# Kernel optimization log

Measured on AMD Instinct MI355X. Metric: run time of the kernel, lower is better.

Reference implementation:

```python
import math
import jax, jax.numpy as jnp
import numpy as np

D_MODEL = 1024
D_STATE = 16
D_CONV = 4
EXPAND = 2
N_MOD = 2
D_INNER = EXPAND * D_MODEL
DT_RANK = math.ceil(D_MODEL / 16)
B_SZ = 2
SEQLEN = 2048


def setup_inputs() -> dict:
    key = jax.random.key(0)
    ks = jax.random.split(key, 10)
    hidden_states = jax.random.normal(ks[0], (B_SZ, SEQLEN, D_MODEL), jnp.float32)
    modality_ids = jax.random.randint(ks[1], (B_SZ, SEQLEN), 0, N_MOD).astype(jnp.int32)
    W_in = jax.random.normal(ks[2], (N_MOD, 2 * D_INNER, D_MODEL), jnp.float32) * (D_MODEL ** -0.5)
    conv_w = jax.random.normal(ks[3], (D_INNER, D_CONV), jnp.float32) * (D_CONV ** -0.5)
    conv_b = jnp.zeros((D_INNER,), jnp.float32)
    W_x = jax.random.normal(ks[4], (N_MOD, DT_RANK + 2 * D_STATE, D_INNER), jnp.float32) * (D_INNER ** -0.5)
    dt_init_std = DT_RANK ** -0.5
    W_dt = jax.random.uniform(ks[5], (N_MOD, D_INNER, DT_RANK), jnp.float32, -dt_init_std, dt_init_std)
    # dt bias init: inverse-softplus of dt ~ LogUniform(dt_min, dt_max), per Mamba
    dt = jnp.exp(jax.random.uniform(ks[6], (N_MOD, D_INNER), jnp.float32)
                 * (math.log(0.1) - math.log(0.001)) + math.log(0.001))
    dt = jnp.maximum(dt, 1e-4)
    b_dt = dt + jnp.log(-jnp.expm1(-dt))
    A_log = jnp.log(jnp.broadcast_to(jnp.arange(1, D_STATE + 1, dtype=jnp.float32), (D_INNER, D_STATE)))
    D = jnp.ones((D_INNER,), jnp.float32)
    W_out = jax.random.normal(ks[7], (N_MOD, D_MODEL, D_INNER), jnp.float32) * (D_INNER ** -0.5)
    return dict(hidden_states=hidden_states, modality_ids=modality_ids, W_in=W_in,
                conv_w=conv_w, conv_b=conv_b, W_x=W_x, W_dt=W_dt, b_dt=b_dt,
                A_log=A_log, D=D, W_out=W_out)


def _expert_apply(x, W, ids):
    # x: [T, d_in], W: [E, d_out, d_in], ids: [T] -> per-token expert output [T, d_out]
    all_out = jnp.einsum('td,eod->teo', x, W)
    return jnp.take_along_axis(all_out, ids[:, None, None], axis=1)[:, 0, :]


def _forward(hidden_states, modality_ids, W_in, conv_w, conv_b, W_x, W_dt, b_dt, A_log, D, W_out):
    Bsz, L, d_model = hidden_states.shape
    d_inner, d_state = A_log.shape
    dt_rank = W_dt.shape[2]
    d_conv = conv_w.shape[1]
    ids = modality_ids.reshape(-1)  # [T]

    # per-modality in_proj dispatch/combine
    xz = _expert_apply(hidden_states.reshape(-1, d_model), W_in, ids)  # [T, 2*d_inner]
    xz = xz.reshape(Bsz, L, 2 * d_inner).transpose(0, 2, 1)            # [B, 2*d_inner, L]
    x, z = jnp.split(xz, 2, axis=1)                                    # [B, d_inner, L] each

    # causal depthwise conv1d (pad left d_conv-1, truncate to L) + SiLU
    xp = jnp.pad(x, ((0, 0), (0, 0), (d_conv - 1, 0)))
    xc = conv_b[None, :, None]
    for k in range(d_conv):
        xc = xc + conv_w[None, :, k:k + 1] * xp[:, :, k:k + L]
    x = jax.nn.silu(xc)

    # per-modality x_proj -> (dt, B, C)
    xt = x.transpose(0, 2, 1).reshape(-1, d_inner)                     # [T, d_inner]
    x_dbl = _expert_apply(xt, W_x, ids)
    dt, Bm, Cm = jnp.split(x_dbl, [dt_rank, dt_rank + d_state], axis=-1)

    # per-modality dt_proj (with bias), then softplus (delta_softplus=True)
    dt = _expert_apply(dt, W_dt, ids) + b_dt[ids]                      # [T, d_inner]
    dt = jax.nn.softplus(dt)

    A = -jnp.exp(A_log)                                                # [d_inner, d_state]

    # selective scan over sequence (time-major)
    dts = dt.reshape(Bsz, L, d_inner).transpose(1, 0, 2)               # [L, B, d_inner]
    Bms = Bm.reshape(Bsz, L, d_state).transpose(1, 0, 2)               # [L, B, d_state]
    Cms = Cm.reshape(Bsz, L, d_state).transpose(1, 0, 2)               # [L, B, d_state]
    xs = x.transpose(2, 0, 1)                                          # [L, B, d_inner]

    def step(state, inp):
        x_t, dt_t, B_t, C_t = inp
        dA = jnp.exp(dt_t[..., None] * A)                              # [B, d_inner, d_state]
        state = state * dA + (dt_t * x_t)[..., None] * B_t[:, None, :]
        y_t = jnp.einsum('bdn,bn->bd', state, C_t)
        return state, y_t

    init = jnp.zeros((Bsz, d_inner, d_state), jnp.float32)
    _, ys = jax.lax.scan(step, init, (xs, dts, Bms, Cms))              # ys: [L, B, d_inner]

    y = ys.transpose(1, 0, 2)                                          # [B, L, d_inner]
    y = y + x.transpose(0, 2, 1) * D[None, None, :]                    # skip D*u
    y = y * jax.nn.silu(z.transpose(0, 2, 1))                          # z gate

    # per-modality out_proj
    out = _expert_apply(y.reshape(-1, d_inner), W_out, ids)
    return out.reshape(Bsz, L, d_model)


def reference(hidden_states, modality_ids, W_in, conv_w, conv_b, W_x, W_dt, b_dt, A_log, D, W_out):
    return _forward(hidden_states, modality_ids, W_in, conv_w, conv_b, W_x, W_dt, b_dt, A_log, D, W_out)
```

## Files before the change

kernel.cpp:

```cpp
#include <hip/hip_runtime.h>
#include <hip/hip_bf16.h>
#include <math.h>

#define B_SZ 2
#define SEQLEN 2048
#define D_MODEL 1024
#define D_INNER 2048
#define D_STATE 16
#define D_CONV 4
#define DT_RANK 64
#define NTOK (B_SZ * SEQLEN)
#define XDBL 96
#define NC 32
#define LC 64
#define PADTOT (17 * 256)

typedef float f32x4 __attribute__((ext_vector_type(4)));
typedef unsigned int u32x4 __attribute__((ext_vector_type(4)));
typedef __hip_bfloat16 bf16;

__device__ __forceinline__ float siluf(float v) { return v / (1.f + __expf(-v)); }
__device__ __forceinline__ float softplusf(float v) {
  return (v > 20.f) ? v : __logf(1.f + __expf(v));
}

__device__ __forceinline__ void mfma_bf16(f32x4& acc, u32x4 a, u32x4 b) {
  asm volatile("v_mfma_f32_16x16x32_bf16 %0, %1, %2, %0" : "+v"(acc) : "v"(a), "v"(b));
}

__device__ __forceinline__ void gload16(const bf16* g, bf16* l) {
  __builtin_amdgcn_global_load_lds(
      (const __attribute__((address_space(1))) unsigned int*)g,
      (__attribute__((address_space(3))) unsigned int*)l, 16, 0, 0);
}

__global__ __launch_bounds__(1024) void k_perm(const int* __restrict__ ids, int* __restrict__ perm) {
  __shared__ int sc[1024];
  const int tid = threadIdx.x;
  int loc[4];
  int cnt = 0;
#pragma unroll
  for (int q = 0; q < 4; q++) {
    loc[q] = ids[tid * 4 + q];
    cnt += (loc[q] == 0);
  }
  sc[tid] = cnt;
  __syncthreads();
  for (int off = 1; off < 1024; off <<= 1) {
    int v = sc[tid];
    int u = (tid >= off) ? sc[tid - off] : 0;
    __syncthreads();
    sc[tid] = v + u;
    __syncthreads();
  }
  const int N0 = sc[1023];
  const int m0 = (N0 + 255) & ~255;
  const int N1 = NTOK - N0;
  for (int idx = tid; idx < PADTOT; idx += 1024)
    if ((idx >= N0 && idx < m0) || idx >= m0 + N1) perm[idx] = -1;
  int zb = sc[tid] - cnt;
#pragma unroll
  for (int q = 0; q < 4; q++) {
    int t = tid * 4 + q;
    if (loc[q] == 0) { perm[zb] = t; zb++; }
    else             { perm[m0 + (t - zb)] = t; }
  }
}

#define CVT_H   (NTOK * D_MODEL)
#define CVT_WIN (2 * 2 * D_INNER * D_MODEL)
#define CVT_WX  (2 * XDBL * D_INNER)
#define CVT_WDT (2 * D_INNER * DT_RANK)
#define CVT_WO  (2 * D_MODEL * D_INNER)
#define CVT_TOT (CVT_H + CVT_WIN + CVT_WX + CVT_WDT + CVT_WO)
__global__ __launch_bounds__(256) void k_cvtall(const float* __restrict__ h,
                                                const float* __restrict__ Win,
                                                const float* __restrict__ Wx,
                                                const float* __restrict__ Wdt,
                                                const float* __restrict__ Wout,
                                                bf16* __restrict__ hB, bf16* __restrict__ WinB,
                                                bf16* __restrict__ WxB, bf16* __restrict__ WdtB,
                                                bf16* __restrict__ WoB) {
  size_t i = ((size_t)blockIdx.x * 256 + threadIdx.x) * 8;
  const float* src; bf16* dst; size_t off;
  if (i < CVT_H)                          { src = h;    dst = hB;   off = i; }
  else if (i < CVT_H + CVT_WIN)           { src = Win;  dst = WinB; off = i - CVT_H; }
  else if (i < CVT_H + CVT_WIN + CVT_WX)  { src = Wx;   dst = WxB;  off = i - CVT_H - CVT_WIN; }
  else if (i < CVT_TOT - CVT_WO)          { src = Wdt;  dst = WdtB; off = i - CVT_H - CVT_WIN - CVT_WX; }
  else                                    { src = Wout; dst = WoB;  off = i - (CVT_TOT - CVT_WO); }
  float4 f0 = *(const float4*)&src[off];
  float4 f1 = *(const float4*)&src[off + 4];
  __align__(16) bf16 tmp[8];
  tmp[0] = __float2bfloat16(f0.x); tmp[1] = __float2bfloat16(f0.y);
  tmp[2] = __float2bfloat16(f0.z); tmp[3] = __float2bfloat16(f0.w);
  tmp[4] = __float2bfloat16(f1.x); tmp[5] = __float2bfloat16(f1.y);
  tmp[6] = __float2bfloat16(f1.z); tmp[7] = __float2bfloat16(f1.w);
  *(u32x4*)&dst[off] = *(const u32x4*)tmp;
}

template <int KDIM, int NW, int KSPLIT, int EPI>
__device__ __forceinline__ void gemmP_body(const bf16* __restrict__ actB,
                                           const int* __restrict__ perm,
                                           const int* __restrict__ ids,
                                           const bf16* __restrict__ WB,
                                           bf16* __restrict__ outx,
                                           bf16* __restrict__ outz,
                                           float* __restrict__ out0) {
  constexpr int KLEN = KDIM / KSPLIT;
  constexpr int NT = KLEN / 64;
  constexpr int NCOL = (EPI == 1) ? (D_MODEL / 128) : 0;
  __shared__ bf16 As[3][256 * 64];
  __shared__ bf16 Ws[3][128 * 64];
  const int tid = threadIdx.x;

  const int gx = gridDim.x;
  const int nwg = gx * gridDim.y;
  const int fid = blockIdx.y * gx + blockIdx.x;
  const int q8 = nwg >> 3;
  const int swz = (fid & 7) * q8 + (fid >> 3);
  const int bx = swz % gx, by = swz / gx;
  const int ot = (KSPLIT > 1) ? (bx % NCOL) * 128 : bx * 128;
  const int kz = (KSPLIT > 1) ? bx / NCOL : 0;
  const int kbase = kz * KLEN;
  const int tt = by * 256;

  const int lane = tid & 63, w = tid >> 6;
  const int wr = w >> 1, wc = w & 1;
  const int lr = lane & 15, lg = lane >> 4;

  const int t00 = perm[tt];
  const int eu = (t00 >= 0) ? ids[t00] : 0;
  const size_t wexp = (size_t)eu * NW * KDIM;

  const int kswz = ((lane & 7) ^ ((lane >> 3) & 7)) * 8;
  size_t aBase[4]; int aLds[4];
  size_t bBase[2]; int bLds[2];
#pragma unroll
  for (int v = 0; v < 4; v++) {
    const int row = w * 32 + v * 8 + (lane >> 3);
    int ta = perm[tt + row]; if (ta < 0) ta = 0;
    aBase[v] = (size_t)ta * KDIM + kswz;
    aLds[v] = (w * 32 + v * 8) * 64;
  }
#pragma unroll
  for (int v = 0; v < 2; v++) {
    const int row = w * 16 + v * 8 + (lane >> 3);
    bBase[v] = wexp + (size_t)(ot + row) * KDIM + kswz;
    bLds[v] = (w * 16 + v * 8) * 64;
  }

  f32x4 acc[4][4];
#pragma unroll
  for (int i = 0; i < 4; i++)
#pragma unroll
    for (int j = 0; j < 4; j++) acc[i][j] = (f32x4){0.f, 0.f, 0.f, 0.f};

#pragma unroll
  for (int kt = 0; kt < 2; kt++) {
    const int k0 = kbase + kt * 64;
    gload16(&actB[aBase[0] + k0], &As[kt][aLds[0]]);
    gload16(&actB[aBase[1] + k0], &As[kt][aLds[1]]);
    gload16(&actB[aBase[2] + k0], &As[kt][aLds[2]]);
    gload16(&actB[aBase[3] + k0], &As[kt][aLds[3]]);
    gload16(&WB[bBase[0] + k0], &Ws[kt][bLds[0]]);
    gload16(&WB[bBase[1] + k0], &Ws[kt][bLds[1]]);
  }

  int bR = 0, bS = 2;
  for (int kt = 0; kt < NT; ++kt) {
    const int kp = kbase + (kt + 2) * 64;
    const bool st = (kt + 2 < NT);
    if (st) {
      gload16(&actB[aBase[0] + kp], &As[bS][aLds[0]]);
      gload16(&actB[aBase[1] + kp], &As[bS][aLds[1]]);
      gload16(&WB[bBase[0] + kp], &Ws[bS][bLds[0]]);
    }
    if (kt < NT - 2)       asm volatile("s_waitcnt vmcnt(9)" ::: "memory");
    else if (kt == NT - 2) asm volatile("s_waitcnt vmcnt(6)" ::: "memory");
    else                   asm volatile("s_waitcnt vmcnt(0)" ::: "memory");
    asm volatile("s_barrier" ::: "memory");

    const bf16* Ab = As[bR];
    const bf16* Wb = Ws[bR];
    u32x4 a[4][2], b0[2][2];
#pragma unroll
    for (int f = 0; f < 4; f++)
#pragma unroll
      for (int s = 0; s < 2; s++) {
        const int row = wr * 64 + f * 16 + lr;
        a[f][s] = *(const u32x4*)&Ab[row * 64 + ((s * 4 + lg) ^ (row & 7)) * 8];
      }
#pragma unroll
    for (int j = 0; j < 2; j++)
#pragma unroll
      for (int s = 0; s < 2; s++) {
        const int row = wc * 64 + j * 16 + lr;
        b0[j][s] = *(const u32x4*)&Wb[row * 64 + ((s * 4 + lg) ^ (row & 7)) * 8];
      }
    __builtin_amdgcn_s_setprio(1);
#pragma unroll
    for (int f = 0; f < 4; f++)
#pragma unroll
      for (int j = 0; j < 2; j++) {
        mfma_bf16(acc[f][j], a[f][0], b0[j][0]);
        mfma_bf16(acc[f][j], a[f][1], b0[j][1]);
      }
    __builtin_amdgcn_s_setprio(0);

    if (st) {
      gload16(&actB[aBase[2] + kp], &As[bS][aLds[2]]);
      gload16(&actB[aBase[3] + kp], &As[bS][aLds[3]]);
      gload16(&WB[bBase[1] + kp], &Ws[bS][bLds[1]]);
    }
    u32x4 b1[2][2];
#pragma unroll
    for (int j = 0; j < 2; j++)
#pragma unroll
      for (int s = 0; s < 2; s++) {
        const int row = wc * 64 + (2 + j) * 16 + lr;
        b1[j][s] = *(const u32x4*)&Wb[row * 64 + ((s * 4 + lg) ^ (row & 7)) * 8];
      }
    __builtin_amdgcn_s_setprio(1);
#pragma unroll
    for (int f = 0; f < 4; f++)
#pragma unroll
      for (int j = 0; j < 2; j++) {
        mfma_bf16(acc[f][2 + j], a[f][0], b1[j][0]);
        mfma_bf16(acc[f][2 + j], a[f][1], b1[j][1]);
      }
    __builtin_amdgcn_s_setprio(0);
    asm volatile("s_waitcnt lgkmcnt(0)" ::: "memory");
    asm volatile("s_barrier" ::: "memory");
    bR = (bR == 2) ? 0 : bR + 1;
    bS = (bS == 2) ? 0 : bS + 1;
  }

#pragma unroll
  for (int i = 0; i < 4; i++) {
#pragma unroll
    for (int r = 0; r < 4; r++) {
      const int m = wr * 64 + i * 16 + lg * 4 + r;
      const int t = perm[tt + m];
      if (t < 0) continue;
#pragma unroll
      for (int j = 0; j < 4; j++) {
        const int col = ot + wc * 64 + j * 16 + lr;
        const float v = acc[i][j][r];
        if (EPI == 0) {
          const bf16 vb = __float2bfloat16(v);
          if (col < D_INNER) outx[(size_t)t * D_INNER + col] = vb;
          else outz[(size_t)t * D_INNER + (col - D_INNER)] = vb;
        } else {
          out0[((size_t)kz * NTOK + t) * D_MODEL + col] = v;
        }
      }
    }
  }
}

__global__ __launch_bounds__(512) void k_inproj(const bf16* actB, const int* perm, const int* ids,
                                                const bf16* WB, bf16* outx, bf16* outz) {
  gemmP_body<D_MODEL, 2 * D_INNER, 1, 0>(actB, perm, ids, WB, outx, outz, nullptr);
}
__global__ __launch_bounds__(512) void k_outproj(const bf16* actB, const int* perm, const int* ids,
                                                 const bf16* WB, float* out0) {
  gemmP_body<D_INNER, D_MODEL, 2, 1>(actB, perm, ids, WB, nullptr, nullptr, out0);
}

__global__ __launch_bounds__(256) void k_xdblg(const bf16* __restrict__ actB,
                                               const int* __restrict__ perm,
                                               const int* __restrict__ ids,
                                               const bf16* __restrict__ WB,
                                               float* __restrict__ out0) {
  constexpr int KDIM = D_INNER, NW = XDBL, LDO = XDBL, KSPLIT = 8;
  constexpr int KLEN = KDIM / KSPLIT;
  __shared__ bf16 As[128 * 64];
  __shared__ bf16 Ws[128 * 64];
  __shared__ int permL[128];
  const int tid = threadIdx.x;
  const int bx = blockIdx.x, by = blockIdx.y;

  const int ot = 0;
  const int kz = bx;
  const int kbase = kz * KLEN;
  const int tt = by * 128;

  if (tid < 128) permL[tid] = perm[tt + tid];

  const int lane = tid & 63, w = tid >> 6;
  const int wr = w >> 1, wc = w & 1;
  const int lr = lane & 15, lg = lane >> 4;

  const int t00 = perm[tt];
  const int eu = (t00 >= 0) ? ids[t00] : 0;
  const size_t wexp = (size_t)eu * NW * KDIM;

  const int srow = w * 32 + (lane >> 3);
  const int scol = (lane & 7) * 8;
  size_t abase[4], bbase[4];
  int ldsoff[4];
#pragma unroll
  for (int v = 0; v < 4; v++) {
    const int row = srow + v * 8;
    int ta = perm[tt + row];
    if (ta < 0) ta = 0;
    abase[v] = (size_t)ta * KDIM + scol;
    int orow = ot + row;
    orow = (orow < NW) ? orow : (NW - 1);
    bbase[v] = wexp + (size_t)orow * KDIM + scol;
    ldsoff[v] = (w * 32 + v * 8) * 64;
  }

  f32x4 acc[4][4];
#pragma unroll
  for (int i = 0; i < 4; i++)
#pragma unroll
    for (int j = 0; j < 4; j++) acc[i][j] = (f32x4){0.f, 0.f, 0.f, 0.f};

  for (int k0 = kbase; k0 < kbase + KLEN; k0 += 64) {
#pragma unroll
    for (int v = 0; v < 4; v++) {
      gload16(&actB[abase[v] + k0], &As[ldsoff[v]]);
      gload16(&WB[bbase[v] + k0], &Ws[ldsoff[v]]);
    }
    __syncthreads();
#pragma unroll
    for (int ks = 0; ks < 64; ks += 32) {
      u32x4 a[4], b[4];
#pragma unroll
      for (int f = 0; f < 4; f++)
        a[f] = *(const u32x4*)&As[(wr * 64 + f * 16 + lr) * 64 + ks + lg * 8];
#pragma unroll
      for (int f = 0; f < 4; f++)
        b[f] = *(const u32x4*)&Ws[(wc * 64 + f * 16 + lr) * 64 + ks + lg * 8];
#pragma unroll
      for (int i = 0; i < 4; i++)
#pragma unroll
        for (int j = 0; j < 4; j++) mfma_bf16(acc[i][j], a[i], b[j]);
    }
    __syncthreads();
  }

#pragma unroll
  for (int i = 0; i < 4; i++) {
#pragma unroll
    for (int r = 0; r < 4; r++) {
      const int m = wr * 64 + i * 16 + lg * 4 + r;
      const int t = permL[m];
      if (t < 0) continue;
#pragma unroll
      for (int j = 0; j < 4; j++) {
        const int col = ot + wc * 64 + j * 16 + lr;
        if (col < NW) out0[((size_t)kz * NTOK + t) * LDO + col] = acc[i][j][r];
      }
    }
  }
}

__global__ __launch_bounds__(256, 4) void k_dtv(const float* __restrict__ xdbl,
                                                const int* __restrict__ perm,
                                                const int* __restrict__ ids,
                                                const float* __restrict__ Wdt,
                                                const float* __restrict__ bdt,
                                                bf16* __restrict__ dtB) {
  __shared__ float Xs[64][65];
  __shared__ float Ws[64][65];
  __shared__ int permL[64];
  const int tid = threadIdx.x;
  const int tt = blockIdx.y * 64;
  const int cb = blockIdx.x * 64;
  if (tid < 64) permL[tid] = perm[tt + tid];
  const int t0 = perm[tt];
  const int e = (t0 >= 0) ? ids[t0] : 0;
  {
    const int r = tid >> 2, q = (tid & 3) * 16;
    int ta = perm[tt + r];
    if (ta < 0) ta = 0;
    const float* xsrc = &xdbl[(size_t)ta * XDBL + q];
    const float* wsrc = &Wdt[((size_t)e * D_INNER + cb + r) * DT_RANK + q];
#pragma unroll
    for (int u = 0; u < 4; u++) {
      float4 xv = *(const float4*)&xsrc[u * 4];
      float4 wv = *(const float4*)&wsrc[u * 4];
      *(float4*)&Xs[r][q + u * 4] = xv;
      *(float4*)&Ws[r][q + u * 4] = wv;
    }
  }
  __syncthreads();
  const int tl = (tid & 15) * 4;
  const int cl = (tid >> 4) * 4;
  float acc[4][4] = {};
#pragma unroll 2
  for (int k4 = 0; k4 < 16; k4++) {
    float4 xv[4], wv[4];
#pragma unroll
    for (int i = 0; i < 4; i++) xv[i] = *(const float4*)&Xs[tl + i][k4 * 4];
#pragma unroll
    for (int j = 0; j < 4; j++) wv[j] = *(const float4*)&Ws[cl + j][k4 * 4];
#pragma unroll
    for (int i = 0; i < 4; i++)
#pragma unroll
      for (int j = 0; j < 4; j++) {
        acc[i][j] = fmaf(xv[i].x, wv[j].x, acc[i][j]);
        acc[i][j] = fmaf(xv[i].y, wv[j].y, acc[i][j]);
        acc[i][j] = fmaf(xv[i].z, wv[j].z, acc[i][j]);
        acc[i][j] = fmaf(xv[i].w, wv[j].w, acc[i][j]);
      }
  }
#pragma unroll
  for (int i = 0; i < 4; i++) {
    const int t = permL[tl + i];
    if (t < 0) continue;
    __align__(8) bf16 ov[4];
#pragma unroll
    for (int j = 0; j < 4; j++)
      ov[j] = __float2bfloat16(softplusf(acc[i][j] + bdt[e * D_INNER + cb + cl + j]));
    *(uint2*)&dtB[(size_t)t * D_INNER + cb + cl] = *(const uint2*)ov;
  }
}

__global__ __launch_bounds__(256) void k_xred(const float* __restrict__ part,
                                              float* __restrict__ xdbl) {
  const int i = blockIdx.x * 256 + threadIdx.x;
  float s = 0.f;
#pragma unroll
  for (int k = 0; k < 8; k++) s += part[(size_t)k * NTOK * XDBL + i];
  xdbl[i] = s;
}

__global__ __launch_bounds__(256) void k_ored2(const float* __restrict__ part,
                                               float* __restrict__ out) {
  const size_t base = ((size_t)blockIdx.x * 256 + threadIdx.x) * 4;
  constexpr size_t NM = (size_t)NTOK * D_MODEL;
  float4 s = *(const float4*)&part[base];
  float4 p = *(const float4*)&part[NM + base];
  s.x += p.x; s.y += p.y; s.z += p.z; s.w += p.w;
  *(float4*)&out[base] = s;
}

__global__ __launch_bounds__(256) void k_conv(const bf16* __restrict__ xrawB,
                                              const float* __restrict__ cw,
                                              const float* __restrict__ cb,
                                              bf16* __restrict__ xB) {
  int idx = blockIdx.x * 256 + threadIdx.x;
  int c = idx & (D_INNER - 1);
  int t = idx >> 11;
  int l = t & (SEQLEN - 1);
  int b = t >> 11;
  float acc = cb[c];
#pragma unroll
  for (int k = 0; k < D_CONV; k++) {
    int ll = l + k - (D_CONV - 1);
    if (ll >= 0)
      acc = fmaf(cw[c * D_CONV + k],
                 __bfloat162float(xrawB[((size_t)(b * SEQLEN + ll)) * D_INNER + c]), acc);
  }
  xB[(size_t)idx] = __float2bfloat16(siluf(acc));
}

__global__ __launch_bounds__(256) void k_scan_part(const bf16* __restrict__ xB,
                                                   const bf16* __restrict__ dtB,
                                                   const float* __restrict__ xdbl,
                                                   const float* __restrict__ A_log,
                                                   float* __restrict__ F,
                                                   float* __restrict__ Sdt) {
  __shared__ float Bs[LC][D_STATE];
  const int tid = threadIdx.x;
  const int j = blockIdx.y;
  const int ch = blockIdx.x * 256 + tid;
  const int b = ch >> 11, c = ch & (D_INNER - 1);
  const int t0 = (b << 11) + j * LC;
  {
    int l = tid >> 2, q = (tid & 3) * 4;
    *(float4*)&Bs[l][q] = *(const float4*)&xdbl[(size_t)(t0 + l) * XDBL + DT_RANK + q];
  }
  float Ar[D_STATE];
#pragma unroll
  for (int n4 = 0; n4 < 4; n4++) {
    float4 a = *(const float4*)&A_log[(size_t)c * D_STATE + n4 * 4];
    Ar[n4 * 4 + 0] = -__expf(a.x); Ar[n4 * 4 + 1] = -__expf(a.y);
    Ar[n4 * 4 + 2] = -__expf(a.z); Ar[n4 * 4 + 3] = -__expf(a.w);
  }
  __syncthreads();
  float st[D_STATE];
#pragma unroll
  for (int n = 0; n < D_STATE; n++) st[n] = 0.f;
  float sdt = 0.f;
  float dtc = __bfloat162float(dtB[(size_t)t0 * D_INNER + c]);
  float xc = __bfloat162float(xB[(size_t)t0 * D_INNER + c]);
  for (int l = 0; l < LC; l++) {
    float dtn = 0.f, xn = 0.f;
    if (l < LC - 1) {
      dtn = __bfloat162float(dtB[(size_t)(t0 + l + 1) * D_INNER + c]);
      xn = __bfloat162float(xB[(size_t)(t0 + l + 1) * D_INNER + c]);
    }
    const float dtx = dtc * xc;
    sdt += dtc;
#pragma unroll
    for (int n = 0; n < D_STATE; n++) {
      float dA = __expf(dtc * Ar[n]);
      st[n] = fmaf(st[n], dA, dtx * Bs[l][n]);
    }
    dtc = dtn; xc = xn;
  }
  const size_t fb = ((size_t)j * NTOK + ch) * D_STATE;
#pragma unroll
  for (int n4 = 0; n4 < 4; n4++)
    *(float4*)&F[fb + n4 * 4] = make_float4(st[n4 * 4], st[n4 * 4 + 1], st[n4 * 4 + 2], st[n4 * 4 + 3]);
  Sdt[(size_t)j * NTOK + ch] = sdt;
}

__global__ __launch_bounds__(256) void k_combine(const float* __restrict__ F,
                                                 const float* __restrict__ Sdt,
                                                 const float* __restrict__ A_log,
                                                 float* __restrict__ s0) {
  const int gid = blockIdx.x * 256 + threadIdx.x;
  const int ch = gid >> 4, n = gid & 15, c = ch & (D_INNER - 1);
  const float Ar = -__expf(A_log[(size_t)c * D_STATE + n]);
  float s = 0.f;
  for (int j = 0; j < NC; j++) {
    s0[((size_t)j * NTOK + ch) * D_STATE + n] = s;
    s = fmaf(s, __expf(Ar * Sdt[(size_t)j * NTOK + ch]), F[((size_t)j * NTOK + ch) * D_STATE + n]);
  }
}

__global__ __launch_bounds__(256) void k_scan_fin(const bf16* __restrict__ xB,
                                                  const bf16* __restrict__ dtB,
                                                  const float* __restrict__ xdbl,
                                                  const bf16* __restrict__ zB,
                                                  const float* __restrict__ A_log,
                                                  const float* __restrict__ Dp,
                                                  const float* __restrict__ s0,
                                                  bf16* __restrict__ ybuf) {
  __shared__ float Bs[LC][D_STATE];
  __shared__ float Cs[LC][D_STATE];
  const int tid = threadIdx.x;
  const int j = blockIdx.y;
  const int ch = blockIdx.x * 256 + tid;
  const int b = ch >> 11, c = ch & (D_INNER - 1);
  const int t0 = (b << 11) + j * LC;
  {
    int l = tid >> 2, q = (tid & 3) * 4;
    *(float4*)&Bs[l][q] = *(const float4*)&xdbl[(size_t)(t0 + l) * XDBL + DT_RANK + q];
    *(float4*)&Cs[l][q] = *(const float4*)&xdbl[(size_t)(t0 + l) * XDBL + DT_RANK + D_STATE + q];
  }
  float Ar[D_STATE];
#pragma unroll
  for (int n4 = 0; n4 < 4; n4++) {
    float4 a = *(const float4*)&A_log[(size_t)c * D_STATE + n4 * 4];
    Ar[n4 * 4 + 0] = -__expf(a.x); Ar[n4 * 4 + 1] = -__expf(a.y);
    Ar[n4 * 4 + 2] = -__expf(a.z); Ar[n4 * 4 + 3] = -__expf(a.w);
  }
  __syncthreads();
  float st[D_STATE];
  const size_t sb = ((size_t)j * NTOK + ch) * D_STATE;
#pragma unroll
  for (int n4 = 0; n4 < 4; n4++) {
    float4 s = *(const float4*)&s0[sb + n4 * 4];
    st[n4 * 4 + 0] = s.x; st[n4 * 4 + 1] = s.y; st[n4 * 4 + 2] = s.z; st[n4 * 4 + 3] = s.w;
  }
  const float Dc = Dp[c];
  float dtc = __bfloat162float(dtB[(size_t)t0 * D_INNER + c]);
  float xc = __bfloat162float(xB[(size_t)t0 * D_INNER + c]);
  for (int l = 0; l < LC; l++) {
    float dtn = 0.f, xn = 0.f;
    if (l < LC - 1) {
      dtn = __bfloat162float(dtB[(size_t)(t0 + l + 1) * D_INNER + c]);
      xn = __bfloat162float(xB[(size_t)(t0 + l + 1) * D_INNER + c]);
    }
    const float zv = __bfloat162float(zB[(size_t)(t0 + l) * D_INNER + c]);
    const float dtx = dtc * xc;
    float y = 0.f;
#pragma unroll
    for (int n = 0; n < D_STATE; n++) {
      float dA = __expf(dtc * Ar[n]);
      st[n] = fmaf(st[n], dA, dtx * Bs[l][n]);
      y = fmaf(st[n], Cs[l][n], y);
    }
    float yv = fmaf(xc, Dc, y);
    ybuf[(size_t)(t0 + l) * D_INNER + c] = __float2bfloat16(yv * siluf(zv));
    dtc = dtn; xc = xn;
  }
}

extern "C" void kernel_launch(void* const* d_in, const int* in_sizes, int n_in,
                              void* d_out, int out_size, void* d_ws, size_t ws_size,
                              hipStream_t stream) {
  const float* h = (const float*)d_in[0];
  const int* ids = (const int*)d_in[1];
  const float* Win = (const float*)d_in[2];
  const float* cw = (const float*)d_in[3];
  const float* cb = (const float*)d_in[4];
  const float* Wx = (const float*)d_in[5];
  const float* Wdt = (const float*)d_in[6];
  const float* bdt = (const float*)d_in[7];
  const float* Alog = (const float*)d_in[8];
  const float* Dp = (const float*)d_in[9];
  const float* Wout = (const float*)d_in[10];
  float* out = (float*)d_out;

  const size_t NTD = (size_t)NTOK * D_INNER;
  float* ws = (float*)d_ws;
  float* slot0 = ws + 0 * NTD;
  float* slot1 = ws + 1 * NTD;
  float* slot2 = ws + 2 * NTD;
  float* slot3 = ws + 3 * NTD;
  size_t cur = 4 * NTD;
  float* xdbl_p = ws + cur; cur += (size_t)NTOK * XDBL;
  float* sdt_p = ws + cur; cur += (size_t)NC * NTOK;
  int* perm = (int*)(ws + cur); cur += PADTOT;
  bf16* xB = (bf16*)(ws + cur); cur += NTD / 2;
  bf16* WoB = (bf16*)(ws + cur); cur += CVT_WO / 2;
  bf16* WxB = (bf16*)(ws + cur); cur += CVT_WX / 2;
  bf16* WdtB = (bf16*)(ws + cur); cur += CVT_WDT / 2;

  bf16* hB = (bf16*)slot0;
  bf16* dtbB = (bf16*)slot0;
  bf16* zB = (bf16*)slot1;
  bf16* WinB = (bf16*)slot2;
  float* part = slot2;
  float* part2 = slot1;
  bf16* xrawB = (bf16*)slot3;
  float* F = slot3;
  bf16* yB = (bf16*)slot3;
  float* s0 = (float*)d_out;

  k_perm<<<1, 1024, 0, stream>>>(ids, perm);
  k_cvtall<<<CVT_TOT / 8 / 256, 256, 0, stream>>>(h, Win, Wx, Wdt, Wout, hB, WinB, WxB, WdtB, WoB);
  k_inproj<<<dim3(32, 17), 512, 0, stream>>>(hB, perm, ids, WinB, xrawB, zB);
  k_conv<<<NTD / 256, 256, 0, stream>>>(xrawB, cw, cb, xB);
  k_xdblg<<<dim3(8, 34), 256, 0, stream>>>(xB, perm, ids, WxB, part);
  k_xred<<<NTOK * XDBL / 256, 256, 0, stream>>>(part, xdbl_p);
  k_dtv<<<dim3(32, PADTOT / 64), 256, 0, stream>>>(xdbl_p, perm, ids, Wdt, bdt, dtbB);
  k_scan_part<<<dim3(16, NC), 256, 0, stream>>>(xB, dtbB, xdbl_p, Alog, F, sdt_p);
  k_combine<<<256, 256, 0, stream>>>(F, sdt_p, Alog, s0);
  k_scan_fin<<<dim3(16, NC), 256, 0, stream>>>(xB, dtbB, xdbl_p, zB, Alog, Dp, s0, yB);
  k_outproj<<<dim3(16, 17), 512, 0, stream>>>(yB, perm, ids, WoB, part2);
  k_ored2<<<NTOK * D_MODEL / 4 / 256, 256, 0, stream>>>(part2, out);
}
```

Before: 321.6 us.

## Specialize out_proj GEMM with 256x256 tiles and store scan chunk states in bf16

The shared templated GEMM is split into a dedicated in_proj kernel and a new out_proj kernel. The out_proj kernel uses 256x256 output tiles, 8 waves arranged 2x4, and double buffering instead of triple, so it launches half as many workgroups and reuses each staged A tile across more columns. Separately, the chunk-final scan states and the combined chunk-start states are written and read as bf16 instead of fp32, halving that intermediate traffic. The bf16 state storage lowers the precision of the carried scan state, and the larger tile raises register and LDS pressure.

```diff
diff --git a/kernel.cpp b/kernel.cpp
--- a/kernel.cpp
+++ b/kernel.cpp
@@ -98,17 +98,15 @@
   *(u32x4*)&dst[off] = *(const u32x4*)tmp;
 }
 
-template <int KDIM, int NW, int KSPLIT, int EPI>
-__device__ __forceinline__ void gemmP_body(const bf16* __restrict__ actB,
-                                           const int* __restrict__ perm,
-                                           const int* __restrict__ ids,
-                                           const bf16* __restrict__ WB,
-                                           bf16* __restrict__ outx,
-                                           bf16* __restrict__ outz,
-                                           float* __restrict__ out0) {
-  constexpr int KLEN = KDIM / KSPLIT;
-  constexpr int NT = KLEN / 64;
-  constexpr int NCOL = (EPI == 1) ? (D_MODEL / 128) : 0;
+__global__ __launch_bounds__(512) void k_inproj(const bf16* __restrict__ actB,
+                                                const int* __restrict__ perm,
+                                                const int* __restrict__ ids,
+                                                const bf16* __restrict__ WB,
+                                                bf16* __restrict__ outx,
+                                                bf16* __restrict__ outz) {
+  constexpr int KDIM = D_MODEL;
+  constexpr int NW = 2 * D_INNER;
+  constexpr int NT = KDIM / 64;
   __shared__ bf16 As[3][256 * 64];
   __shared__ bf16 Ws[3][128 * 64];
   const int tid = threadIdx.x;
@@ -119,9 +117,7 @@
   const int q8 = nwg >> 3;
   const int swz = (fid & 7) * q8 + (fid >> 3);
   const int bx = swz % gx, by = swz / gx;
-  const int ot = (KSPLIT > 1) ? (bx % NCOL) * 128 : bx * 128;
-  const int kz = (KSPLIT > 1) ? bx / NCOL : 0;
-  const int kbase = kz * KLEN;
+  const int ot = bx * 128;
   const int tt = by * 256;
 
   const int lane = tid & 63, w = tid >> 6;
@@ -157,7 +153,7 @@
 
 #pragma unroll
   for (int kt = 0; kt < 2; kt++) {
-    const int k0 = kbase + kt * 64;
+    const int k0 = kt * 64;
     gload16(&actB[aBase[0] + k0], &As[kt][aLds[0]]);
     gload16(&actB[aBase[1] + k0], &As[kt][aLds[1]]);
     gload16(&actB[aBase[2] + k0], &As[kt][aLds[2]]);
@@ -168,7 +164,7 @@
 
   int bR = 0, bS = 2;
   for (int kt = 0; kt < NT; ++kt) {
-    const int kp = kbase + (kt + 2) * 64;
+    const int kp = (kt + 2) * 64;
     const bool st = (kt + 2 < NT);
     if (st) {
       gload16(&actB[aBase[0] + kp], &As[bS][aLds[0]]);
@@ -245,26 +241,127 @@
 #pragma unroll
       for (int j = 0; j < 4; j++) {
         const int col = ot + wc * 64 + j * 16 + lr;
-        const float v = acc[i][j][r];
-        if (EPI == 0) {
-          const bf16 vb = __float2bfloat16(v);
-          if (col < D_INNER) outx[(size_t)t * D_INNER + col] = vb;
-          else outz[(size_t)t * D_INNER + (col - D_INNER)] = vb;
-        } else {
-          out0[((size_t)kz * NTOK + t) * D_MODEL + col] = v;
-        }
-      }
-    }
-  }
-}
-
-__global__ __launch_bounds__(512) void k_inproj(const bf16* actB, const int* perm, const int* ids,
-                                                const bf16* WB, bf16* outx, bf16* outz) {
-  gemmP_body<D_MODEL, 2 * D_INNER, 1, 0>(actB, perm, ids, WB, outx, outz, nullptr);
-}
-__global__ __launch_bounds__(512) void k_outproj(const bf16* actB, const int* perm, const int* ids,
-                                                 const bf16* WB, float* out0) {
-  gemmP_body<D_INNER, D_MODEL, 2, 1>(actB, perm, ids, WB, nullptr, nullptr, out0);
+        const bf16 v = __float2bfloat16(acc[i][j][r]);
+        if (col < D_INNER) outx[(size_t)t * D_INNER + col] = v;
+        else outz[(size_t)t * D_INNER + (col - D_INNER)] = v;
+      }
+    }
+  }
+}
+
+__global__ __launch_bounds__(512) void k_outproj(const bf16* __restrict__ actB,
+                                                 const int* __restrict__ perm,
+                                                 const int* __restrict__ ids,
+                                                 const bf16* __restrict__ WB,
+                                                 float* __restrict__ out0) {
+  constexpr int KDIM = D_INNER;
+  constexpr int NW = D_MODEL;
+  constexpr int KSPLIT = 2;
+  constexpr int KLEN = KDIM / KSPLIT;
+  constexpr int NT = KLEN / 64;
+  constexpr int NCOL = NW / 256;
+  __shared__ bf16 As[2][256 * 64];
+  __shared__ bf16 Ws[2][256 * 64];
+  const int tid = threadIdx.x;
+
+  const int gx = gridDim.x;
+  const int nwg = gx * gridDim.y;
+  const int fid = blockIdx.y * gx + blockIdx.x;
+  const int q8 = nwg >> 3;
+  const int swz = (fid & 7) * q8 + (fid >> 3);
+  const int bx = swz % gx, by = swz / gx;
+  const int ot = (bx % NCOL) * 256;
+  const int kz = bx / NCOL;
+  const int kbase = kz * KLEN;
+  const int tt = by * 256;
+
+  const int lane = tid & 63, w = tid >> 6;
+  const int wr = w >> 2, wc = w & 3;
+  const int lr = lane & 15, lg = lane >> 4;
+
+  const int t00 = perm[tt];
+  const int eu = (t00 >= 0) ? ids[t00] : 0;
+  const size_t wexp = (size_t)eu * NW * KDIM;
+
+  const int srow_l = lane >> 3;
+  const int kswz = ((lane & 7) ^ srow_l) * 8;
+  size_t aBase[4], bBase[4];
+  int ldsE[4];
+#pragma unroll
+  for (int v = 0; v < 4; v++) {
+    const int row = (w * 4 + v) * 8 + srow_l;
+    int ta = perm[tt + row];
+    if (ta < 0) ta = 0;
+    aBase[v] = (size_t)ta * KDIM + kswz;
+    bBase[v] = wexp + (size_t)(ot + row) * KDIM + kswz;
+    ldsE[v] = (w * 4 + v) * 512;
+  }
+
+  f32x4 acc[8][4];
+#pragma unroll
+  for (int i = 0; i < 8; i++)
+#pragma unroll
+    for (int j = 0; j < 4; j++) acc[i][j] = (f32x4){0.f, 0.f, 0.f, 0.f};
+
+  auto STAGE = [&](int buf, int k0) {
+#pragma unroll
+    for (int v = 0; v < 4; v++) {
+      gload16(&actB[aBase[v] + k0], &As[buf][ldsE[v]]);
+      gload16(&WB[bBase[v] + k0], &Ws[buf][ldsE[v]]);
+    }
+  };
+
+  STAGE(0, kbase);
+  int cur = 0;
+  for (int kt = 0; kt < NT; ++kt) {
+    if (kt + 1 < NT) {
+      STAGE(cur ^ 1, kbase + (kt + 1) * 64);
+      asm volatile("s_waitcnt vmcnt(8)" ::: "memory");
+    } else {
+      asm volatile("s_waitcnt vmcnt(0)" ::: "memory");
+    }
+    asm volatile("s_barrier" ::: "memory");
+    const bf16* Ab = As[cur];
+    const bf16* Wb = Ws[cur];
+#pragma unroll
+    for (int s = 0; s < 2; s++) {
+      u32x4 a[8], b[4];
+#pragma unroll
+      for (int f = 0; f < 8; f++) {
+        const int row = wr * 128 + f * 16 + lr;
+        a[f] = *(const u32x4*)&Ab[row * 64 + ((s * 4 + lg) ^ (row & 7)) * 8];
+      }
+#pragma unroll
+      for (int j = 0; j < 4; j++) {
+        const int row = wc * 64 + j * 16 + lr;
+        b[j] = *(const u32x4*)&Wb[row * 64 + ((s * 4 + lg) ^ (row & 7)) * 8];
+      }
+      __builtin_amdgcn_s_setprio(1);
+#pragma unroll
+      for (int f = 0; f < 8; f++)
+#pragma unroll
+        for (int j = 0; j < 4; j++) mfma_bf16(acc[f][j], a[f], b[j]);
+      __builtin_amdgcn_s_setprio(0);
+    }
+    asm volatile("s_waitcnt lgkmcnt(0)" ::: "memory");
+    asm volatile("s_barrier" ::: "memory");
+    cur ^= 1;
+  }
+
+#pragma unroll
+  for (int i = 0; i < 8; i++) {
+#pragma unroll
+    for (int r = 0; r < 4; r++) {
+      const int m = wr * 128 + i * 16 + lg * 4 + r;
+      const int t = perm[tt + m];
+      if (t < 0) continue;
+#pragma unroll
+      for (int j = 0; j < 4; j++) {
+        const int col = ot + wc * 64 + j * 16 + lr;
+        out0[((size_t)kz * NTOK + t) * D_MODEL + col] = acc[i][j][r];
+      }
+    }
+  }
 }
 
 __global__ __launch_bounds__(256) void k_xdblg(const bf16* __restrict__ actB,
@@ -462,7 +559,7 @@
                                                    const bf16* __restrict__ dtB,
                                                    const float* __restrict__ xdbl,
                                                    const float* __restrict__ A_log,
-                                                   float* __restrict__ F,
+                                                   bf16* __restrict__ F,
                                                    float* __restrict__ Sdt) {
   __shared__ float Bs[LC][D_STATE];
   const int tid = threadIdx.x;
@@ -504,23 +601,26 @@
     dtc = dtn; xc = xn;
   }
   const size_t fb = ((size_t)j * NTOK + ch) * D_STATE;
-#pragma unroll
-  for (int n4 = 0; n4 < 4; n4++)
-    *(float4*)&F[fb + n4 * 4] = make_float4(st[n4 * 4], st[n4 * 4 + 1], st[n4 * 4 + 2], st[n4 * 4 + 3]);
+  __align__(16) bf16 fv[16];
+#pragma unroll
+  for (int n = 0; n < D_STATE; n++) fv[n] = __float2bfloat16(st[n]);
+  *(u32x4*)&F[fb] = *(const u32x4*)fv;
+  *(u32x4*)&F[fb + 8] = *(const u32x4*)(fv + 8);
   Sdt[(size_t)j * NTOK + ch] = sdt;
 }
 
-__global__ __launch_bounds__(256) void k_combine(const float* __restrict__ F,
+__global__ __launch_bounds__(256) void k_combine(const bf16* __restrict__ F,
                                                  const float* __restrict__ Sdt,
                                                  const float* __restrict__ A_log,
-                                                 float* __restrict__ s0) {
+                                                 bf16* __restrict__ s0) {
   const int gid = blockIdx.x * 256 + threadIdx.x;
   const int ch = gid >> 4, n = gid & 15, c = ch & (D_INNER - 1);
   const float Ar = -__expf(A_log[(size_t)c * D_STATE + n]);
   float s = 0.f;
   for (int j = 0; j < NC; j++) {
-    s0[((size_t)j * NTOK + ch) * D_STATE + n] = s;
-    s = fmaf(s, __expf(Ar * Sdt[(size_t)j * NTOK + ch]), F[((size_t)j * NTOK + ch) * D_STATE + n]);
+    s0[((size_t)j * NTOK + ch) * D_STATE + n] = __float2bfloat16(s);
+    s = fmaf(s, __expf(Ar * Sdt[(size_t)j * NTOK + ch]),
+             __bfloat162float(F[((size_t)j * NTOK + ch) * D_STATE + n]));
   }
 }
 
@@ -530,7 +630,7 @@
                                                   const bf16* __restrict__ zB,
                                                   const float* __restrict__ A_log,
                                                   const float* __restrict__ Dp,
-                                                  const float* __restrict__ s0,
+                                                  const bf16* __restrict__ s0,
                                                   bf16* __restrict__ ybuf) {
   __shared__ float Bs[LC][D_STATE];
   __shared__ float Cs[LC][D_STATE];
@@ -555,10 +655,7 @@
   float st[D_STATE];
   const size_t sb = ((size_t)j * NTOK + ch) * D_STATE;
 #pragma unroll
-  for (int n4 = 0; n4 < 4; n4++) {
-    float4 s = *(const float4*)&s0[sb + n4 * 4];
-    st[n4 * 4 + 0] = s.x; st[n4 * 4 + 1] = s.y; st[n4 * 4 + 2] = s.z; st[n4 * 4 + 3] = s.w;
-  }
+  for (int n = 0; n < D_STATE; n++) st[n] = __bfloat162float(s0[sb + n]);
   const float Dc = Dp[c];
   float dtc = __bfloat162float(dtB[(size_t)t0 * D_INNER + c]);
   float xc = __bfloat162float(xB[(size_t)t0 * D_INNER + c]);
@@ -621,9 +718,9 @@
   float* part = slot2;
   float* part2 = slot1;
   bf16* xrawB = (bf16*)slot3;
-  float* F = slot3;
+  bf16* F = (bf16*)slot3;
   bf16* yB = (bf16*)slot3;
-  float* s0 = (float*)d_out;
+  bf16* s0 = (bf16*)d_out;
 
   k_perm<<<1, 1024, 0, stream>>>(ids, perm);
   k_cvtall<<<CVT_TOT / 8 / 256, 256, 0, stream>>>(h, Win, Wx, Wdt, Wout, hB, WinB, WxB, WdtB, WoB);
@@ -635,6 +732,6 @@
   k_scan_part<<<dim3(16, NC), 256, 0, stream>>>(xB, dtbB, xdbl_p, Alog, F, sdt_p);
   k_combine<<<256, 256, 0, stream>>>(F, sdt_p, Alog, s0);
   k_scan_fin<<<dim3(16, NC), 256, 0, stream>>>(xB, dtbB, xdbl_p, zB, Alog, Dp, s0, yB);
-  k_outproj<<<dim3(16, 17), 512, 0, stream>>>(yB, perm, ids, WoB, part2);
+  k_outproj<<<dim3(8, 17), 512, 0, stream>>>(yB, perm, ids, WoB, part2);
   k_ored2<<<NTOK * D_MODEL / 4 / 256, 256, 0, stream>>>(part2, out);
 }
```

Result: faster. 307.9 us (-4.2%).
